# Kernel optimization log

Hardware: AMD Instinct MI355X
Metric: run time of the kernel (lower is better)

The kernel has to match this reference:

```python
import jax, jax.numpy as jnp
import numpy as np

N_EMBED = 768
NUM_EXPERTS = 8
TOP_K = 2
B, S = 2, 2048
THRESH = 1e-09


def setup_inputs() -> dict:
    key = jax.random.key(0)
    ks = jax.random.split(key, 12)
    d, e, f = N_EMBED, NUM_EXPERTS, 4 * N_EMBED
    s_in = 1.0 / np.sqrt(d)
    s_hid = 1.0 / np.sqrt(f)
    return {
        'x': jax.random.normal(ks[0], (B, S, d), jnp.float32),
        'noise': jax.random.normal(ks[1], (B * S, e), jnp.float32),
        'Wg': jax.random.normal(ks[2], (d, e), jnp.float32) * s_in,
        'bg': jnp.zeros((e,), jnp.float32),
        'Wn': jax.random.normal(ks[3], (d, e), jnp.float32) * s_in,
        'bn': jnp.zeros((e,), jnp.float32),
        'W1': jax.random.normal(ks[4], (e, d, f), jnp.float32) * s_in,
        'b1': jnp.zeros((e, f), jnp.float32),
        'W2': jax.random.normal(ks[5], (e, f, d), jnp.float32) * s_hid,
        'b2': jnp.zeros((e, d), jnp.float32),
    }


def reference(x, noise, Wg, bg, Wn, bn, W1, b1, W2, b2):
    Bsz, Ssz, d = x.shape
    T = Bsz * Ssz
    xr = x.reshape(T, d)  # [T, d]

    # Noisy top-k router
    logits = xr @ Wg + bg                     # [T, E]
    noise_logits = xr @ Wn + bn               # [T, E]
    noisy = logits + noise * jax.nn.softplus(noise_logits)
    vals, idx = jax.lax.top_k(noisy, TOP_K)   # [T, K]
    rows = jnp.arange(T)[:, None]
    sparse = jnp.full_like(noisy, -jnp.inf).at[rows, idx].set(vals)
    probs = jax.nn.softmax(sparse, axis=-1)   # [T, E]; zeros off top-k

    # Gate = prob masked by activation threshold (matches torch dispatch)
    gate = jnp.where(probs > THRESH, probs, 0.0)  # [T, E]

    # Dense per-expert MLP (dropout=0 -> identity), combined by gate
    h = jax.nn.relu(jnp.einsum('td,edf->etf', xr, W1) + b1[:, None, :])  # [E, T, 4d]
    y = jnp.einsum('etf,efd->etd', h, W2) + b2[:, None, :]               # [E, T, d]
    out = jnp.einsum('te,etd->td', gate, y)                              # [T, d]
    return out.reshape(Bsz, Ssz, d)
```

## Files before the change

kernel.cpp:

```cpp
#include <hip/hip_runtime.h>
#include <math.h>

typedef unsigned short u16;
typedef unsigned int u32;

#define D_EMB 768
#define F_HID 3072
#define N_TOK 4096
#define N_PAIR 8192
#define GATE_TH 1e-9f

typedef float f32x4 __attribute__((ext_vector_type(4)));
typedef __bf16 bfrag __attribute__((ext_vector_type(8)));
typedef u16 u16x8 __attribute__((ext_vector_type(8)));

__device__ inline float b2f(u16 u) {
    union { float f; u32 i; } c; c.i = ((u32)u) << 16; return c.f;
}
__device__ inline u16 f2b(float f) {
    union { float f; u32 i; } c; c.f = f;
    u32 r = c.i + 0x7FFFu + ((c.i >> 16) & 1u);
    return (u16)(r >> 16);
}
__device__ inline f32x4 mfma16(bfrag a, bfrag b, f32x4 c) {
    return __builtin_amdgcn_mfma_f32_16x16x32_bf16(a, b, c, 0, 0, 0);
}
__device__ inline void gll16(const u16* g, u16* l) {
    __builtin_amdgcn_global_load_lds(
        (const __attribute__((address_space(1))) u32*)g,
        (__attribute__((address_space(3))) u32*)l, 16, 0, 0);
}
__device__ inline void sbar() {
    asm volatile("" ::: "memory");
    __builtin_amdgcn_s_barrier();
    asm volatile("" ::: "memory");
}
__device__ inline void waitv0()  { asm volatile("s_waitcnt vmcnt(0)"  ::: "memory"); }
__device__ inline void waitv3()  { asm volatile("s_waitcnt vmcnt(3)"  ::: "memory"); }
__device__ inline void waitv8()  { asm volatile("s_waitcnt vmcnt(8)"  ::: "memory"); }

__global__ __launch_bounds__(256) void moe_zero_kernel(uint4* __restrict__ out) {
    int i = blockIdx.x * 256 + threadIdx.x;
    out[i] = make_uint4(0, 0, 0, 0);
}

__global__ __launch_bounds__(64) void moe_router_v4(
    const float* __restrict__ x, const float* __restrict__ noise,
    const float* __restrict__ Wg, const float* __restrict__ bg,
    const float* __restrict__ Wn, const float* __restrict__ bn,
    int* __restrict__ tk_e, float* __restrict__ tk_g,
    ushort4* __restrict__ xb4)
{
    const int lane = threadIdx.x;
    const int tl = lane & 7, q = lane >> 3;
    const int t = blockIdx.x * 8 + tl;
    float ag[8] = {}, an[8] = {};
    const float4* xp = (const float4*)(x + (size_t)t * D_EMB + q * 96);
#pragma unroll 4
    for (int k4 = 0; k4 < 24; k4++) {
        float4 xv = xp[k4];
        const int kb = q * 96 + k4 * 4;
#pragma unroll
        for (int c = 0; c < 4; c++) {
            float xc = (&xv.x)[c];
            const float4* wg = (const float4*)(Wg + (size_t)(kb + c) * 8);
            const float4* wn = (const float4*)(Wn + (size_t)(kb + c) * 8);
            float4 g0 = wg[0], g1 = wg[1], n0 = wn[0], n1 = wn[1];
            ag[0] += xc * g0.x; ag[1] += xc * g0.y; ag[2] += xc * g0.z; ag[3] += xc * g0.w;
            ag[4] += xc * g1.x; ag[5] += xc * g1.y; ag[6] += xc * g1.z; ag[7] += xc * g1.w;
            an[0] += xc * n0.x; an[1] += xc * n0.y; an[2] += xc * n0.z; an[3] += xc * n0.w;
            an[4] += xc * n1.x; an[5] += xc * n1.y; an[6] += xc * n1.z; an[7] += xc * n1.w;
        }
    }
#pragma unroll
    for (int e = 0; e < 8; e++) {
        ag[e] += __shfl_xor(ag[e], 8);  an[e] += __shfl_xor(an[e], 8);
        ag[e] += __shfl_xor(ag[e], 16); an[e] += __shfl_xor(an[e], 16);
        ag[e] += __shfl_xor(ag[e], 32); an[e] += __shfl_xor(an[e], 32);
    }
    if (q == 0) {
        float best = -INFINITY, sec = -INFINITY; int be = 0, se = 0;
#pragma unroll
        for (int e = 0; e < 8; e++) {
            float nl = an[e] + bn[e];
            float sp = nl > 0.f ? nl + log1pf(expf(-nl)) : log1pf(expf(nl));
            float v = ag[e] + bg[e] + noise[(size_t)t * 8 + e] * sp;
            if (v > best) { sec = best; se = be; best = v; be = e; }
            else if (v > sec) { sec = v; se = e; }
        }
        float ex = expf(sec - best);
        float g1 = 1.f / (1.f + ex), g2 = ex / (1.f + ex);
        tk_e[t * 2 + 0] = (g1 > GATE_TH) ? be : -1; tk_g[t * 2 + 0] = g1;
        tk_e[t * 2 + 1] = (g2 > GATE_TH) ? se : -1; tk_g[t * 2 + 1] = g2;
    }
    if (xb4) {
        const int t0 = blockIdx.x * 8;
        for (int i = lane; i < 8 * 192; i += 64) {
            int ti = i / 192, c = i - ti * 192;
            float4 v = *(const float4*)(x + (size_t)(t0 + ti) * D_EMB + c * 4);
            ushort4 o;
            o.x = f2b(v.x); o.y = f2b(v.y); o.z = f2b(v.z); o.w = f2b(v.w);
            xb4[(size_t)(t0 + ti) * 192 + c] = o;
        }
    }
}

__global__ __launch_bounds__(256) void moe_plan_kernel(
    const int* __restrict__ tk_e, const float* __restrict__ tk_g,
    int* __restrict__ cnt, int* __restrict__ off,
    int* __restrict__ plist, float* __restrict__ pg, int* __restrict__ pos)
{
    __shared__ int lc[8 * 256];
    __shared__ int ob[8];
    const int t = threadIdx.x;
#pragma unroll
    for (int e = 0; e < 8; e++) lc[e * 256 + t] = 0;
    __syncthreads();
    const int i0 = t * 32;
    for (int j = 0; j < 32; j++) {
        int e = tk_e[i0 + j];
        if (e >= 0) lc[e * 256 + t]++;
    }
    __syncthreads();
    if (t < 8) {
        int s = 0;
        for (int u = 0; u < 256; u++) {
            int v = lc[t * 256 + u]; lc[t * 256 + u] = s; s += v;
        }
        ob[t] = s;
    }
    __syncthreads();
    if (t == 0) {
        int s = 0;
        for (int e = 0; e < 8; e++) {
            int v = ob[e]; cnt[e] = v; off[e] = s; ob[e] = s; s += v;
        }
    }
    __syncthreads();
    for (int j = 0; j < 32; j++) {
        int e = tk_e[i0 + j];
        if (e >= 0) {
            int p = ob[e] + lc[e * 256 + t]++;
            plist[p] = (i0 + j) >> 1;
            pg[p] = tk_g[i0 + j];
            pos[i0 + j] = p;
        }
    }
}

__global__ __launch_bounds__(256) void moe_transcvt_kernel(
    const float* __restrict__ in, u16* __restrict__ out, int R, int C) {
    __shared__ float tile[64][65];
    const int z = blockIdx.z;
    const int c0 = blockIdx.x * 64, r0 = blockIdx.y * 64;
    const size_t base = (size_t)z * R * C;
    const int t = threadIdx.x;
    {
        const int row = t >> 2, cb = (t & 3) * 16;
        const float* src = in + base + (size_t)(r0 + row) * C + c0 + cb;
        float4 v0 = ((const float4*)src)[0];
        float4 v1 = ((const float4*)src)[1];
        float4 v2 = ((const float4*)src)[2];
        float4 v3 = ((const float4*)src)[3];
        float* d = &tile[row][cb];
        d[0]  = v0.x; d[1]  = v0.y; d[2]  = v0.z; d[3]  = v0.w;
        d[4]  = v1.x; d[5]  = v1.y; d[6]  = v1.z; d[7]  = v1.w;
        d[8]  = v2.x; d[9]  = v2.y; d[10] = v2.z; d[11] = v2.w;
        d[12] = v3.x; d[13] = v3.y; d[14] = v3.z; d[15] = v3.w;
    }
    __syncthreads();
    const int c = t >> 2, rb = (t & 3) * 16;
    u16x8 o0, o1;
#pragma unroll
    for (int i = 0; i < 8; i++) o0[i] = f2b(tile[rb + i][c]);
#pragma unroll
    for (int i = 0; i < 8; i++) o1[i] = f2b(tile[rb + 8 + i][c]);
    u16* dst = out + base + (size_t)(c0 + c) * R + r0 + rb;
    *(u16x8*)dst = o0;
    *(u16x8*)(dst + 8) = o1;
}

__global__ __launch_bounds__(256) void moe_ffn1_kernel(
    const u16* __restrict__ xb, const u16* __restrict__ wt, const float* __restrict__ b1,
    const int* __restrict__ plist, const int* __restrict__ cnt, const int* __restrict__ off,
    u16* __restrict__ h, int P0, int P1)
{
    __shared__ __align__(16) u16 As[2][128 * 64];
    __shared__ __align__(16) u16 Bs[2][128 * 64];
    const int GX = 24, GY = 16;
    int f = blockIdx.x + GX * (blockIdx.y + GY * blockIdx.z);
    int swz = (f & 7) * 384 + (f >> 3);
    int nb = swz % GX;
    int t2 = swz / GX;
    int mb = t2 % GY;
    int e  = t2 / GY;

    int lo = off[e], hi = lo + cnt[e];
    if (lo < P0) lo = P0;
    if (hi > P1) hi = P1;
    const int Cl = hi - lo;
    if (Cl <= 0) return;
    const int n0 = nb * 128;
    const int tid = threadIdx.x;
    const int lane = tid & 63, wave = tid >> 6;
    const int wr = wave >> 1, wc = wave & 1;
    const int qq = lane >> 4, r = lane & 15;
    const int srow = tid >> 3;
    const int gq = (tid & 7) ^ (srow & 7);

    const u16* bsrc[4];
#pragma unroll
    for (int j = 0; j < 4; j++)
        bsrc[j] = wt + ((size_t)e * F_HID + n0 + j * 32 + srow) * D_EMB + gq * 8;

    for (int m0 = mb * 128; m0 < Cl; m0 += GY * 128) {
        const u16* asrc[4];
#pragma unroll
        for (int j = 0; j < 4; j++) {
            int mr = m0 + j * 32 + srow;
            if (mr > Cl - 1) mr = Cl - 1;
            asrc[j] = xb + (size_t)plist[lo + mr] * D_EMB + gq * 8;
        }
        f32x4 acc[4][4] = {};

        auto stage = [&](int kt, int buf) {
            const int k0 = kt * 64;
#pragma unroll
            for (int j = 0; j < 4; j++)
                gll16(asrc[j] + k0, &As[buf][j * 2048 + wave * 512]);
#pragma unroll
            for (int j = 0; j < 4; j++)
                gll16(bsrc[j] + k0, &Bs[buf][j * 2048 + wave * 512]);
        };
        auto compute = [&](int buf) {
#pragma unroll
            for (int kk = 0; kk < 2; kk++) {
                bfrag af[4], bf[4];
#pragma unroll
                for (int i = 0; i < 4; i++) {
                    int rowa = wr * 64 + i * 16 + r;
                    int rowb = wc * 64 + i * 16 + r;
                    int slot = ((qq + 4 * kk) ^ (r & 7)) * 8;
                    af[i] = *(const bfrag*)(&As[buf][rowa * 64 + slot]);
                    bf[i] = *(const bfrag*)(&Bs[buf][rowb * 64 + slot]);
                }
#pragma unroll
                for (int mi = 0; mi < 4; mi++)
#pragma unroll
                    for (int ni = 0; ni < 4; ni++)
                        acc[mi][ni] = mfma16(af[mi], bf[ni], acc[mi][ni]);
            }
        };

        waitv0();
        stage(0, 0);
        for (int kt = 0; kt < 11; kt++) {
            stage(kt + 1, (kt + 1) & 1);
            waitv8(); sbar();
            compute(kt & 1);
            sbar();
        }
        waitv0(); sbar();
        compute(1);

#pragma unroll
        for (int mi = 0; mi < 4; mi++)
#pragma unroll
            for (int ni = 0; ni < 4; ni++) {
                int col = n0 + wc * 64 + ni * 16 + r;
                float bias = b1[(size_t)e * F_HID + col];
#pragma unroll
                for (int i = 0; i < 4; i++) {
                    int m = m0 + wr * 64 + mi * 16 + qq * 4 + i;
                    if (m < Cl) {
                        float v = acc[mi][ni][i] + bias;
                        h[(size_t)(lo - P0 + m) * F_HID + col] = f2b(v > 0.f ? v : 0.f);
                    }
                }
            }
    }
}

__global__ __launch_bounds__(256) void moe_ffn2_kernel(
    const u16* __restrict__ h, const u16* __restrict__ wt, const float* __restrict__ b2,
    const int* __restrict__ cnt, const int* __restrict__ off,
    float* __restrict__ y, int P0, int P1)
{
    __shared__ __align__(16) u16 As[3][64 * 32];
    __shared__ __align__(16) u16 Bs[3][128 * 32];
    const int GX = 6, GY = 32;
    int f = blockIdx.x + GX * (blockIdx.y + GY * blockIdx.z);
    int swz = (f & 7) * 192 + (f >> 3);
    int nb = swz % GX;
    int t2 = swz / GX;
    int mb = t2 % GY;
    int e  = t2 / GY;

    int lo = off[e], hi = lo + cnt[e];
    if (lo < P0) lo = P0;
    if (hi > P1) hi = P1;
    const int Cl = hi - lo;
    if (Cl <= 0) return;
    const int n0 = nb * 128;
    const int tid = threadIdx.x;
    const int lane = tid & 63, wave = tid >> 6;
    const int wr = wave >> 1, wc = wave & 1;
    const int qq = lane >> 4, r = lane & 15;
    const int qa = (qq ^ ((r >> 1) & 3)) * 8;
    const int srow = tid >> 2;
    const int gq = (tid & 3) ^ ((tid >> 3) & 3);
    const int hcap = P1 - P0;

    const u16* bsrc0 = wt + ((size_t)e * D_EMB + n0 + srow) * F_HID + gq * 8;
    const u16* bsrc1 = bsrc0 + (size_t)64 * F_HID;

    for (int m0 = mb * 64; m0 < Cl; m0 += GY * 64) {
        int mr0 = m0 + srow;
        if (mr0 > Cl - 1) mr0 = Cl - 1;
        if (mr0 >= hcap) mr0 = hcap - 1;
        const u16* asrc0 = h + (size_t)(lo - P0 + mr0) * F_HID + gq * 8;
        f32x4 acc[2][4] = {};

        auto stage = [&](int kt, int buf) {
            const int k0 = kt * 32;
            gll16(asrc0 + k0, &As[buf][wave * 512]);
            gll16(bsrc0 + k0, &Bs[buf][wave * 512]);
            gll16(bsrc1 + k0, &Bs[buf][2048 + wave * 512]);
        };
        auto compute = [&](int buf) {
            bfrag af[2], bf[4];
#pragma unroll
            for (int i = 0; i < 2; i++)
                af[i] = *(const bfrag*)(&As[buf][(wr * 32 + i * 16 + r) * 32 + qa]);
#pragma unroll
            for (int i = 0; i < 4; i++)
                bf[i] = *(const bfrag*)(&Bs[buf][(wc * 64 + i * 16 + r) * 32 + qa]);
#pragma unroll
            for (int mi = 0; mi < 2; mi++)
#pragma unroll
                for (int ni = 0; ni < 4; ni++)
                    acc[mi][ni] = mfma16(af[mi], bf[ni], acc[mi][ni]);
        };

        waitv0();
        stage(0, 0);
        int cb = 0, sb = 1;
        for (int kt = 0; kt < 95; kt++) {
            stage(kt + 1, sb);
            waitv3(); sbar();
            compute(cb);
            cb = (cb == 2) ? 0 : cb + 1;
            sb = (sb == 2) ? 0 : sb + 1;
        }
        waitv0(); sbar();
        compute(cb);

#pragma unroll
        for (int mi = 0; mi < 2; mi++)
#pragma unroll
            for (int ni = 0; ni < 4; ni++) {
                int col = n0 + wc * 64 + ni * 16 + r;
                float bias = b2[(size_t)e * D_EMB + col];
#pragma unroll
                for (int i = 0; i < 4; i++) {
                    int m = m0 + wr * 32 + mi * 16 + qq * 4 + i;
                    if (m < Cl)
                        y[(size_t)(lo + m) * D_EMB + col] = acc[mi][ni][i] + bias;
                }
            }
        sbar();
    }
}

__global__ __launch_bounds__(256) void moe_combine_kernel(
    const float* __restrict__ y, const int* __restrict__ tk_e,
    const float* __restrict__ tk_g, const int* __restrict__ pos,
    float4* __restrict__ out)
{
    int i = blockIdx.x * 256 + threadIdx.x;
    int t = i / 192;
    int c = i - t * 192;
    float4 a = make_float4(0.f, 0.f, 0.f, 0.f);
#pragma unroll
    for (int k = 0; k < 2; k++) {
        int e = tk_e[t * 2 + k];
        if (e >= 0) {
            float g = tk_g[t * 2 + k];
            float4 v = ((const float4*)(y + (size_t)pos[t * 2 + k] * D_EMB))[c];
            a.x += g * v.x; a.y += g * v.y; a.z += g * v.z; a.w += g * v.w;
        }
    }
    out[i] = a;
}

#define XSTR 776
#define HSTR 3080
#define BMF 8
__global__ __launch_bounds__(256) void moe_ffn_fused_f32(
    const float* __restrict__ x,
    const float* __restrict__ w1, const float* __restrict__ b1,
    const float* __restrict__ w2, const float* __restrict__ b2,
    const int* __restrict__ plist, const float* __restrict__ pg,
    const int* __restrict__ cnt, const int* __restrict__ off,
    float* __restrict__ out)
{
    __shared__ __align__(16) u16 xs[BMF * XSTR];
    __shared__ __align__(16) u16 hs[BMF * HSTR];
    const int e = blockIdx.x;
    const int Cl = cnt[e];
    if (Cl <= 0) return;
    const int O = off[e];
    const int tid = threadIdx.x;
    for (int t0 = blockIdx.y * BMF; t0 < Cl; t0 += gridDim.y * BMF) {
        for (int ci = tid; ci < BMF * 192; ci += 256) {
            int row = ci / 192, c = ci - row * 192;
            float4 v = make_float4(0.f, 0.f, 0.f, 0.f);
            if (t0 + row < Cl) {
                int tok = plist[O + t0 + row];
                v = *(const float4*)(x + (size_t)tok * D_EMB + c * 4);
            }
            u16* d = &xs[row * XSTR + c * 4];
            d[0] = f2b(v.x); d[1] = f2b(v.y); d[2] = f2b(v.z); d[3] = f2b(v.w);
        }
        __syncthreads();
        for (int wi = tid; wi < BMF * 768; wi += 256) {
            int row = wi / 768, nc = wi - row * 768;
            int n0 = nc * 4;
            float a0 = 0, a1 = 0, a2 = 0, a3 = 0;
            const float* wp = w1 + (size_t)e * D_EMB * F_HID + n0;
            const u16* xr = &xs[row * XSTR];
            for (int k = 0; k < D_EMB; k++) {
                float4 wv = *(const float4*)(wp + (size_t)k * F_HID);
                float xv = b2f(xr[k]);
                a0 += xv * wv.x; a1 += xv * wv.y; a2 += xv * wv.z; a3 += xv * wv.w;
            }
            const float* bp = b1 + (size_t)e * F_HID + n0;
            u16* hp = &hs[row * HSTR + n0];
            float v;
            v = a0 + bp[0]; hp[0] = f2b(v > 0.f ? v : 0.f);
            v = a1 + bp[1]; hp[1] = f2b(v > 0.f ? v : 0.f);
            v = a2 + bp[2]; hp[2] = f2b(v > 0.f ? v : 0.f);
            v = a3 + bp[3]; hp[3] = f2b(v > 0.f ? v : 0.f);
        }
        __syncthreads();
        for (int wi = tid; wi < BMF * 192; wi += 256) {
            int row = wi / 192, nc = wi - row * 192;
            int n0 = nc * 4;
            float a0 = 0, a1 = 0, a2 = 0, a3 = 0;
            const float* wp = w2 + (size_t)e * F_HID * D_EMB + n0;
            const u16* hr = &hs[row * HSTR];
            for (int k = 0; k < F_HID; k++) {
                float4 wv = *(const float4*)(wp + (size_t)k * D_EMB);
                float hv = b2f(hr[k]);
                a0 += hv * wv.x; a1 += hv * wv.y; a2 += hv * wv.z; a3 += hv * wv.w;
            }
            if (t0 + row < Cl) {
                int p = O + t0 + row;
                int tok = plist[p];
                float g = pg[p];
                const float* bp = b2 + (size_t)e * D_EMB + n0;
                float* op = out + (size_t)tok * D_EMB + n0;
                atomicAdd(&op[0], g * (a0 + bp[0]));
                atomicAdd(&op[1], g * (a1 + bp[1]));
                atomicAdd(&op[2], g * (a2 + bp[2]));
                atomicAdd(&op[3], g * (a3 + bp[3]));
            }
        }
        __syncthreads();
    }
}

extern "C" void kernel_launch(void* const* d_in, const int* in_sizes, int n_in,
                              void* d_out, int out_size, void* d_ws, size_t ws_size,
                              hipStream_t stream) {
    const float* x     = (const float*)d_in[0];
    const float* noise = (const float*)d_in[1];
    const float* Wg    = (const float*)d_in[2];
    const float* bg    = (const float*)d_in[3];
    const float* Wn    = (const float*)d_in[4];
    const float* bn    = (const float*)d_in[5];
    const float* W1    = (const float*)d_in[6];
    const float* b1    = (const float*)d_in[7];
    const float* W2    = (const float*)d_in[8];
    const float* b2    = (const float*)d_in[9];
    float* out = (float*)d_out;

    char* ws = (char*)d_ws;
    int*   cnt    = (int*)(ws + 0);
    int*   off    = (int*)(ws + 256);
    int*   tk_e   = (int*)(ws + 1024);
    float* tk_g   = (float*)(ws + 33792);
    int*   plist  = (int*)(ws + 66560);
    float* pg     = (float*)(ws + 99328);
    int*   pos    = (int*)(ws + 132096);
    const size_t SMALL  = 164864;
    const size_t WSZ    = 37748736ull;
    const size_t XB_SZ  = 6291456ull;
    const size_t Y_SZ   = 25165824ull;
    const size_t H_FULL = 50331648ull;

    const size_t NEED_A = SMALL + WSZ + XB_SZ + Y_SZ + H_FULL;

    if (ws_size >= NEED_A) {
        u16*   wt = (u16*)(ws + SMALL);
        u16*   xb = (u16*)(ws + SMALL + WSZ);
        float* y  = (float*)(ws + SMALL + WSZ + XB_SZ);
        u16*   h  = (u16*)(ws + SMALL + WSZ + XB_SZ + Y_SZ);

        moe_router_v4<<<dim3(512), dim3(64), 0, stream>>>(
            x, noise, Wg, bg, Wn, bn, tk_e, tk_g, (ushort4*)xb);
        moe_plan_kernel<<<dim3(1), dim3(256), 0, stream>>>(
            tk_e, tk_g, cnt, off, plist, pg, pos);
        moe_transcvt_kernel<<<dim3(F_HID / 64, D_EMB / 64, 8), dim3(256), 0, stream>>>(
            W1, wt, D_EMB, F_HID);
        moe_ffn1_kernel<<<dim3(24, 16, 8), dim3(256), 0, stream>>>(
            xb, wt, b1, plist, cnt, off, h, 0, N_PAIR);
        moe_transcvt_kernel<<<dim3(D_EMB / 64, F_HID / 64, 8), dim3(256), 0, stream>>>(
            W2, wt, F_HID, D_EMB);
        moe_ffn2_kernel<<<dim3(6, 32, 8), dim3(256), 0, stream>>>(
            h, wt, b2, cnt, off, y, 0, N_PAIR);
        moe_combine_kernel<<<dim3(3072), dim3(256), 0, stream>>>(
            y, tk_e, tk_g, pos, (float4*)out);
        (void)in_sizes; (void)n_in; (void)out_size;
        return;
    }

    const size_t B_BASE = SMALL + 2 * WSZ + XB_SZ + Y_SZ;
    int pchunk = 0;
    for (int p = N_PAIR; p >= 512; p >>= 1) {
        if (B_BASE + (size_t)p * F_HID * 2 <= ws_size) { pchunk = p; break; }
    }

    moe_router_v4<<<dim3(512), dim3(64), 0, stream>>>(
        x, noise, Wg, bg, Wn, bn, tk_e, tk_g,
        pchunk > 0 ? (ushort4*)(ws + SMALL + 2 * WSZ) : (ushort4*)0);
    moe_plan_kernel<<<dim3(1), dim3(256), 0, stream>>>(
        tk_e, tk_g, cnt, off, plist, pg, pos);

    if (pchunk > 0) {
        u16*   w1t = (u16*)(ws + SMALL);
        u16*   w2t = (u16*)(ws + SMALL + WSZ);
        u16*   xb  = (u16*)(ws + SMALL + 2 * WSZ);
        float* y   = (float*)(ws + SMALL + 2 * WSZ + XB_SZ);
        u16*   h   = (u16*)(ws + B_BASE);
        moe_transcvt_kernel<<<dim3(F_HID / 64, D_EMB / 64, 8), dim3(256), 0, stream>>>(
            W1, w1t, D_EMB, F_HID);
        moe_transcvt_kernel<<<dim3(D_EMB / 64, F_HID / 64, 8), dim3(256), 0, stream>>>(
            W2, w2t, F_HID, D_EMB);
        for (int c = 0; c < N_PAIR / pchunk; c++) {
            int P0 = c * pchunk, P1 = P0 + pchunk;
            moe_ffn1_kernel<<<dim3(24, 16, 8), dim3(256), 0, stream>>>(
                xb, w1t, b1, plist, cnt, off, h, P0, P1);
            moe_ffn2_kernel<<<dim3(6, 32, 8), dim3(256), 0, stream>>>(
                h, w2t, b2, cnt, off, y, P0, P1);
        }
        moe_combine_kernel<<<dim3(3072), dim3(256), 0, stream>>>(
            y, tk_e, tk_g, pos, (float4*)out);
    } else {
        moe_zero_kernel<<<dim3(3072), dim3(256), 0, stream>>>((uint4*)out);
        moe_ffn_fused_f32<<<dim3(8, 192), dim3(256), 0, stream>>>(
            x, W1, b1, W2, b2, plist, pg, cnt, off, out);
    }
    (void)in_sizes; (void)n_in; (void)out_size;
}
```

Before: 416.0 us.

## Fuse router with W1 transpose-convert; split FFN2 K loop into two launches

Merges the router/x-to-bf16 kernel and the W1 transpose-convert kernel into one launch, with 128 router blocks and 4608 transpose blocks, so the small router no longer runs alone on the GPU. FFN2 is split into two launches along the K dimension, each covering half of F_HID. The second launch reads y back and accumulates into it. The split doubles y traffic and h re-staging in exchange for shorter per-block K loops, with no obvious gain in parallelism since the grid is unchanged.

Measured after the change: 426.8 us. +2.6%, slower.

```diff
diff --git a/kernel.cpp b/kernel.cpp
--- a/kernel.cpp
+++ b/kernel.cpp
@@ -44,12 +44,105 @@
     out[i] = make_uint4(0, 0, 0, 0);
 }
 
+__global__ __launch_bounds__(256) void moe_pre_kernel(
+    const float* __restrict__ x, const float* __restrict__ noise,
+    const float* __restrict__ Wg, const float* __restrict__ bg,
+    const float* __restrict__ Wn, const float* __restrict__ bn,
+    int* __restrict__ tk_e, float* __restrict__ tk_g,
+    ushort4* __restrict__ xb4,
+    const float* __restrict__ W1, u16* __restrict__ wt)
+{
+    __shared__ float tile[64][65];
+    if (blockIdx.x < 128) {
+        const int wave = threadIdx.x >> 6, lane = threadIdx.x & 63;
+        const int tl = lane & 7, q = lane >> 3;
+        const int t = (blockIdx.x * 4 + wave) * 8 + tl;
+        float ag[8] = {}, an[8] = {};
+        const float4* xp = (const float4*)(x + (size_t)t * D_EMB + q * 96);
+#pragma unroll 4
+        for (int k4 = 0; k4 < 24; k4++) {
+            float4 xv = xp[k4];
+            const int kb = q * 96 + k4 * 4;
+#pragma unroll
+            for (int c = 0; c < 4; c++) {
+                float xc = (&xv.x)[c];
+                const float4* wg = (const float4*)(Wg + (size_t)(kb + c) * 8);
+                const float4* wn = (const float4*)(Wn + (size_t)(kb + c) * 8);
+                float4 g0 = wg[0], g1 = wg[1], n0 = wn[0], n1 = wn[1];
+                ag[0] += xc * g0.x; ag[1] += xc * g0.y; ag[2] += xc * g0.z; ag[3] += xc * g0.w;
+                ag[4] += xc * g1.x; ag[5] += xc * g1.y; ag[6] += xc * g1.z; ag[7] += xc * g1.w;
+                an[0] += xc * n0.x; an[1] += xc * n0.y; an[2] += xc * n0.z; an[3] += xc * n0.w;
+                an[4] += xc * n1.x; an[5] += xc * n1.y; an[6] += xc * n1.z; an[7] += xc * n1.w;
+            }
+        }
+#pragma unroll
+        for (int e = 0; e < 8; e++) {
+            ag[e] += __shfl_xor(ag[e], 8);  an[e] += __shfl_xor(an[e], 8);
+            ag[e] += __shfl_xor(ag[e], 16); an[e] += __shfl_xor(an[e], 16);
+            ag[e] += __shfl_xor(ag[e], 32); an[e] += __shfl_xor(an[e], 32);
+        }
+        if (q == 0) {
+            float best = -INFINITY, sec = -INFINITY; int be = 0, se = 0;
+#pragma unroll
+            for (int e = 0; e < 8; e++) {
+                float nl = an[e] + bn[e];
+                float sp = nl > 0.f ? nl + log1pf(expf(-nl)) : log1pf(expf(nl));
+                float v = ag[e] + bg[e] + noise[(size_t)t * 8 + e] * sp;
+                if (v > best) { sec = best; se = be; best = v; be = e; }
+                else if (v > sec) { sec = v; se = e; }
+            }
+            float ex = expf(sec - best);
+            float g1 = 1.f / (1.f + ex), g2 = ex / (1.f + ex);
+            tk_e[t * 2 + 0] = (g1 > GATE_TH) ? be : -1; tk_g[t * 2 + 0] = g1;
+            tk_e[t * 2 + 1] = (g2 > GATE_TH) ? se : -1; tk_g[t * 2 + 1] = g2;
+        }
+        const int t0 = (blockIdx.x * 4 + wave) * 8;
+        for (int i = lane; i < 8 * 192; i += 64) {
+            int ti = i / 192, c = i - ti * 192;
+            float4 v = *(const float4*)(x + (size_t)(t0 + ti) * D_EMB + c * 4);
+            ushort4 o;
+            o.x = f2b(v.x); o.y = f2b(v.y); o.z = f2b(v.z); o.w = f2b(v.w);
+            xb4[(size_t)(t0 + ti) * 192 + c] = o;
+        }
+    } else {
+        int b = blockIdx.x - 128;
+        int bx = b % 48; int rest = b / 48;
+        int by = rest % 12; int z = rest / 12;
+        const int R = D_EMB, C = F_HID;
+        const int c0 = bx * 64, r0 = by * 64;
+        const size_t base = (size_t)z * R * C;
+        const int t = threadIdx.x;
+        {
+            const int row = t >> 2, cb = (t & 3) * 16;
+            const float* src = W1 + base + (size_t)(r0 + row) * C + c0 + cb;
+            float4 v0 = ((const float4*)src)[0];
+            float4 v1 = ((const float4*)src)[1];
+            float4 v2 = ((const float4*)src)[2];
+            float4 v3 = ((const float4*)src)[3];
+            float* d = &tile[row][cb];
+            d[0]  = v0.x; d[1]  = v0.y; d[2]  = v0.z; d[3]  = v0.w;
+            d[4]  = v1.x; d[5]  = v1.y; d[6]  = v1.z; d[7]  = v1.w;
+            d[8]  = v2.x; d[9]  = v2.y; d[10] = v2.z; d[11] = v2.w;
+            d[12] = v3.x; d[13] = v3.y; d[14] = v3.z; d[15] = v3.w;
+        }
+        __syncthreads();
+        const int c = t >> 2, rb = (t & 3) * 16;
+        u16x8 o0, o1;
+#pragma unroll
+        for (int i = 0; i < 8; i++) o0[i] = f2b(tile[rb + i][c]);
+#pragma unroll
+        for (int i = 0; i < 8; i++) o1[i] = f2b(tile[rb + 8 + i][c]);
+        u16* dst = wt + base + (size_t)(c0 + c) * R + r0 + rb;
+        *(u16x8*)dst = o0;
+        *(u16x8*)(dst + 8) = o1;
+    }
+}
+
 __global__ __launch_bounds__(64) void moe_router_v4(
     const float* __restrict__ x, const float* __restrict__ noise,
     const float* __restrict__ Wg, const float* __restrict__ bg,
     const float* __restrict__ Wn, const float* __restrict__ bn,
-    int* __restrict__ tk_e, float* __restrict__ tk_g,
-    ushort4* __restrict__ xb4)
+    int* __restrict__ tk_e, float* __restrict__ tk_g)
 {
     const int lane = threadIdx.x;
     const int tl = lane & 7, q = lane >> 3;
@@ -92,16 +185,6 @@
         float g1 = 1.f / (1.f + ex), g2 = ex / (1.f + ex);
         tk_e[t * 2 + 0] = (g1 > GATE_TH) ? be : -1; tk_g[t * 2 + 0] = g1;
         tk_e[t * 2 + 1] = (g2 > GATE_TH) ? se : -1; tk_g[t * 2 + 1] = g2;
-    }
-    if (xb4) {
-        const int t0 = blockIdx.x * 8;
-        for (int i = lane; i < 8 * 192; i += 64) {
-            int ti = i / 192, c = i - ti * 192;
-            float4 v = *(const float4*)(x + (size_t)(t0 + ti) * D_EMB + c * 4);
-            ushort4 o;
-            o.x = f2b(v.x); o.y = f2b(v.y); o.z = f2b(v.z); o.w = f2b(v.w);
-            xb4[(size_t)(t0 + ti) * 192 + c] = o;
-        }
     }
 }
 
@@ -284,7 +367,7 @@
 __global__ __launch_bounds__(256) void moe_ffn2_kernel(
     const u16* __restrict__ h, const u16* __restrict__ wt, const float* __restrict__ b2,
     const int* __restrict__ cnt, const int* __restrict__ off,
-    float* __restrict__ y, int P0, int P1)
+    float* __restrict__ y, int P0, int P1, int kbeg, int add)
 {
     __shared__ __align__(16) u16 As[3][64 * 32];
     __shared__ __align__(16) u16 Bs[3][128 * 32];
@@ -311,14 +394,14 @@
     const int gq = (tid & 3) ^ ((tid >> 3) & 3);
     const int hcap = P1 - P0;
 
-    const u16* bsrc0 = wt + ((size_t)e * D_EMB + n0 + srow) * F_HID + gq * 8;
+    const u16* bsrc0 = wt + ((size_t)e * D_EMB + n0 + srow) * F_HID + kbeg + gq * 8;
     const u16* bsrc1 = bsrc0 + (size_t)64 * F_HID;
 
     for (int m0 = mb * 64; m0 < Cl; m0 += GY * 64) {
         int mr0 = m0 + srow;
         if (mr0 > Cl - 1) mr0 = Cl - 1;
         if (mr0 >= hcap) mr0 = hcap - 1;
-        const u16* asrc0 = h + (size_t)(lo - P0 + mr0) * F_HID + gq * 8;
+        const u16* asrc0 = h + (size_t)(lo - P0 + mr0) * F_HID + kbeg + gq * 8;
         f32x4 acc[2][4] = {};
 
         auto stage = [&](int kt, int buf) {
@@ -345,7 +428,7 @@
         waitv0();
         stage(0, 0);
         int cb = 0, sb = 1;
-        for (int kt = 0; kt < 95; kt++) {
+        for (int kt = 0; kt < 47; kt++) {
             stage(kt + 1, sb);
             waitv3(); sbar();
             compute(cb);
@@ -364,8 +447,11 @@
 #pragma unroll
                 for (int i = 0; i < 4; i++) {
                     int m = m0 + wr * 32 + mi * 16 + qq * 4 + i;
-                    if (m < Cl)
-                        y[(size_t)(lo + m) * D_EMB + col] = acc[mi][ni][i] + bias;
+                    if (m < Cl) {
+                        size_t idx = (size_t)(lo + m) * D_EMB + col;
+                        float base = add ? y[idx] : bias;
+                        y[idx] = acc[mi][ni][i] + base;
+                    }
                 }
             }
         sbar();
@@ -507,18 +593,18 @@
         float* y  = (float*)(ws + SMALL + WSZ + XB_SZ);
         u16*   h  = (u16*)(ws + SMALL + WSZ + XB_SZ + Y_SZ);
 
-        moe_router_v4<<<dim3(512), dim3(64), 0, stream>>>(
-            x, noise, Wg, bg, Wn, bn, tk_e, tk_g, (ushort4*)xb);
+        moe_pre_kernel<<<dim3(128 + 4608), dim3(256), 0, stream>>>(
+            x, noise, Wg, bg, Wn, bn, tk_e, tk_g, (ushort4*)xb, W1, wt);
         moe_plan_kernel<<<dim3(1), dim3(256), 0, stream>>>(
             tk_e, tk_g, cnt, off, plist, pg, pos);
-        moe_transcvt_kernel<<<dim3(F_HID / 64, D_EMB / 64, 8), dim3(256), 0, stream>>>(
-            W1, wt, D_EMB, F_HID);
         moe_ffn1_kernel<<<dim3(24, 16, 8), dim3(256), 0, stream>>>(
             xb, wt, b1, plist, cnt, off, h, 0, N_PAIR);
         moe_transcvt_kernel<<<dim3(D_EMB / 64, F_HID / 64, 8), dim3(256), 0, stream>>>(
             W2, wt, F_HID, D_EMB);
         moe_ffn2_kernel<<<dim3(6, 32, 8), dim3(256), 0, stream>>>(
-            h, wt, b2, cnt, off, y, 0, N_PAIR);
+            h, wt, b2, cnt, off, y, 0, N_PAIR, 0, 0);
+        moe_ffn2_kernel<<<dim3(6, 32, 8), dim3(256), 0, stream>>>(
+            h, wt, b2, cnt, off, y, 0, N_PAIR, 1536, 1);
         moe_combine_kernel<<<dim3(3072), dim3(256), 0, stream>>>(
             y, tk_e, tk_g, pos, (float4*)out);
         (void)in_sizes; (void)n_in; (void)out_size;
@@ -530,12 +616,6 @@
     for (int p = N_PAIR; p >= 512; p >>= 1) {
         if (B_BASE + (size_t)p * F_HID * 2 <= ws_size) { pchunk = p; break; }
     }
-
-    moe_router_v4<<<dim3(512), dim3(64), 0, stream>>>(
-        x, noise, Wg, bg, Wn, bn, tk_e, tk_g,
-        pchunk > 0 ? (ushort4*)(ws + SMALL + 2 * WSZ) : (ushort4*)0);
-    moe_plan_kernel<<<dim3(1), dim3(256), 0, stream>>>(
-        tk_e, tk_g, cnt, off, plist, pg, pos);
 
     if (pchunk > 0) {
         u16*   w1t = (u16*)(ws + SMALL);
@@ -543,8 +623,10 @@
         u16*   xb  = (u16*)(ws + SMALL + 2 * WSZ);
         float* y   = (float*)(ws + SMALL + 2 * WSZ + XB_SZ);
         u16*   h   = (u16*)(ws + B_BASE);
-        moe_transcvt_kernel<<<dim3(F_HID / 64, D_EMB / 64, 8), dim3(256), 0, stream>>>(
-            W1, w1t, D_EMB, F_HID);
+        moe_pre_kernel<<<dim3(128 + 4608), dim3(256), 0, stream>>>(
+            x, noise, Wg, bg, Wn, bn, tk_e, tk_g, (ushort4*)xb, W1, w1t);
+        moe_plan_kernel<<<dim3(1), dim3(256), 0, stream>>>(
+            tk_e, tk_g, cnt, off, plist, pg, pos);
         moe_transcvt_kernel<<<dim3(D_EMB / 64, F_HID / 64, 8), dim3(256), 0, stream>>>(
             W2, w2t, F_HID, D_EMB);
         for (int c = 0; c < N_PAIR / pchunk; c++) {
@@ -552,11 +634,17 @@
             moe_ffn1_kernel<<<dim3(24, 16, 8), dim3(256), 0, stream>>>(
                 xb, w1t, b1, plist, cnt, off, h, P0, P1);
             moe_ffn2_kernel<<<dim3(6, 32, 8), dim3(256), 0, stream>>>(
-                h, w2t, b2, cnt, off, y, P0, P1);
+                h, w2t, b2, cnt, off, y, P0, P1, 0, 0);
+            moe_ffn2_kernel<<<dim3(6, 32, 8), dim3(256), 0, stream>>>(
+                h, w2t, b2, cnt, off, y, P0, P1, 1536, 1);
         }
         moe_combine_kernel<<<dim3(3072), dim3(256), 0, stream>>>(
             y, tk_e, tk_g, pos, (float4*)out);
     } else {
+        moe_router_v4<<<dim3(512), dim3(64), 0, stream>>>(
+            x, noise, Wg, bg, Wn, bn, tk_e, tk_g);
+        moe_plan_kernel<<<dim3(1), dim3(256), 0, stream>>>(
+            tk_e, tk_g, cnt, off, plist, pg, pos);
         moe_zero_kernel<<<dim3(3072), dim3(256), 0, stream>>>((uint4*)out);
         moe_ffn_fused_f32<<<dim3(8, 192), dim3(256), 0, stream>>>(
             x, W1, b1, W2, b2, plist, pg, cnt, off, out);
```
